# Optimization experiments

Hardware: AMD Instinct MI355X
Metric: run time of the kernel (lower is better)

Reference implementation:

```python
import jax, jax.numpy as jnp
import numpy as np

B, S, H, I, E, K = 2, 2048, 896, 4864, 4, 2


def setup_inputs() -> dict:
    key = jax.random.key(0)
    ks = jax.random.split(key, 5)
    s_h = 1.0 / np.sqrt(H)
    s_i = 1.0 / np.sqrt(I)
    return {
        "x": jax.random.normal(ks[0], (B, S, H), dtype=jnp.float32),
        # torch nn.Linear weights are [out, in]
        "router_w": jax.random.uniform(ks[1], (E, H), dtype=jnp.float32, minval=-s_h, maxval=s_h),
        "gate_w": jax.random.uniform(ks[2], (E, I, H), dtype=jnp.float32, minval=-s_h, maxval=s_h),
        "up_w": jax.random.uniform(ks[3], (E, I, H), dtype=jnp.float32, minval=-s_h, maxval=s_h),
        "down_w": jax.random.uniform(ks[4], (E, H, I), dtype=jnp.float32, minval=-s_i, maxval=s_i),
    }


def reference(x, router_w, gate_w, up_w, down_w):
    # Router: softmax in fp32, top-k, renormalize (matches torch.softmax(dtype=float) + topk)
    logits = jnp.einsum("bsh,eh->bse", x, router_w)
    probs = jax.nn.softmax(logits.astype(jnp.float32), axis=-1)
    top_w, top_i = jax.lax.top_k(probs, K)                      # [B,S,K]
    top_w = top_w / jnp.sum(top_w, axis=-1, keepdims=True)
    # Dense per-expert combine weight: zero for unselected experts
    w_full = jnp.sum(jax.nn.one_hot(top_i, E, dtype=x.dtype) * top_w[..., None].astype(x.dtype), axis=-2)  # [B,S,E]
    # All experts on all tokens (E is small); unselected get weight 0
    gate = jax.nn.silu(jnp.einsum("bsh,eih->bsei", x, gate_w))  # [B,S,E,I]
    up = jnp.einsum("bsh,eih->bsei", x, up_w)
    y = jnp.einsum("bsei,ehi->bseh", gate * up, down_w)          # [B,S,E,H]
    return jnp.einsum("bseh,bse->bsh", y, w_full)
```

## Files before the change

kernel.cpp:

```cpp
#include <hip/hip_runtime.h>
#include <hip/hip_bf16.h>

#define E_ 4
#define H_ 896
#define I_ 4864
#define T_ 4096
#define P_ 8192
#define KS2 2432

typedef unsigned short u16;
typedef __attribute__((ext_vector_type(8))) short short8;
typedef __attribute__((ext_vector_type(4))) float f32x4;

__device__ __forceinline__ void gload16(const void* g, void* l) {
  __builtin_amdgcn_global_load_lds(
      (const __attribute__((address_space(1))) unsigned int*)g,
      (__attribute__((address_space(3))) unsigned int*)l, 16, 0, 0);
}

__device__ __forceinline__ u16 f2bf(float f) {
  unsigned int u = __builtin_bit_cast(unsigned int, f);
  unsigned int r = (u + 0x7FFFu + ((u >> 16) & 1u)) >> 16;
  return (u16)r;
}

__global__ __launch_bounds__(256) void cast_bf16_kernel(const float* __restrict__ in,
                                                        u16* __restrict__ out, long n) {
  long base = ((long)blockIdx.x * 256 + threadIdx.x) * 4;
  if (base + 3 < n) {
    float4 v = *reinterpret_cast<const float4*>(in + base);
    ushort4 o;
    o.x = f2bf(v.x); o.y = f2bf(v.y); o.z = f2bf(v.z); o.w = f2bf(v.w);
    *reinterpret_cast<ushort4*>(out + base) = o;
  } else {
    for (long j = base; j < n; ++j) out[j] = f2bf(in[j]);
  }
}

__global__ __launch_bounds__(64) void router_kernel(const float* __restrict__ x,
                                                    const float* __restrict__ rw,
                                                    int* __restrict__ cnt,
                                                    int* __restrict__ pairs,
                                                    float* __restrict__ wgt) {
  int t = blockIdx.x;
  int lane = threadIdx.x;
  const float* xr = x + (long)t * H_;
  float a0 = 0.f, a1 = 0.f, a2 = 0.f, a3 = 0.f;
  for (int h = lane; h < H_; h += 64) {
    float xv = xr[h];
    a0 += xv * rw[0 * H_ + h];
    a1 += xv * rw[1 * H_ + h];
    a2 += xv * rw[2 * H_ + h];
    a3 += xv * rw[3 * H_ + h];
  }
  for (int off = 32; off > 0; off >>= 1) {
    a0 += __shfl_xor(a0, off, 64);
    a1 += __shfl_xor(a1, off, 64);
    a2 += __shfl_xor(a2, off, 64);
    a3 += __shfl_xor(a3, off, 64);
  }
  if (lane == 0) {
    float l[4] = {a0, a1, a2, a3};
    int i0 = 0;
    for (int e = 1; e < 4; ++e) if (l[e] > l[i0]) i0 = e;
    int i1 = -1;
    for (int e = 0; e < 4; ++e) {
      if (e == i0) continue;
      if (i1 < 0 || l[e] > l[i1]) i1 = e;
    }
    float w0 = 1.0f / (1.0f + __expf(l[i1] - l[i0]));
    int j0 = atomicAdd(&cnt[i0], 1);
    pairs[i0 * T_ + j0] = 2 * t;
    wgt[2 * t] = w0;
    int j1 = atomicAdd(&cnt[i1], 1);
    pairs[i1 * T_ + j1] = 2 * t + 1;
    wgt[2 * t + 1] = 1.0f - w0;
  }
}


__global__ __launch_bounds__(256, 2) void gemm1_kernel(const u16* __restrict__ xb,
                                                       const u16* __restrict__ gw,
                                                       const u16* __restrict__ uw,
                                                       const int* __restrict__ cnt,
                                                       const int* __restrict__ pairs,
                                                       u16* __restrict__ hbuf) {
  int e = blockIdx.z;
  int n = cnt[e];
  int row0 = blockIdx.y * 128;
  if (row0 >= n) return;
  int col0 = blockIdx.x * 128;

  __shared__ alignas(16) u16 As[128 * 64];
  __shared__ alignas(16) u16 Bg[128 * 64];
  __shared__ alignas(16) u16 Bu[128 * 64];
  __shared__ int rows[128];

  int tid = threadIdx.x;
  if (tid < 128) {
    int j = row0 + tid;
    if (j >= n) j = n - 1;
    rows[tid] = pairs[e * T_ + j];
  }
  __syncthreads();

  int rr = tid >> 3;
  int cc = tid & 7;
  long eoff = (long)e * I_ * H_;

  const u16* aP[4]; const u16* gP[4]; const u16* uP[4];
  u16* lA[4]; u16* lG[4]; u16* lU[4];
#pragma unroll
  for (int q = 0; q < 4; ++q) {
    int gr = rr + 32 * q;
    int g8 = (cc ^ (gr & 7)) * 8;
    aP[q] = xb + (long)(rows[gr] >> 1) * H_ + g8;
    gP[q] = gw + eoff + (long)(col0 + gr) * H_ + g8;
    uP[q] = uw + eoff + (long)(col0 + gr) * H_ + g8;
    lA[q] = As + q * 2048 + tid * 8;
    lG[q] = Bg + q * 2048 + tid * 8;
    lU[q] = Bu + q * 2048 + tid * 8;
  }

  f32x4 accg[4][4] = {};
  f32x4 accu[4][4] = {};

  int lane = tid & 63;
  int wave = tid >> 6;
  int wm = (wave >> 1) * 64;
  int wn = (wave & 1) * 64;
  int lm = lane & 15;
  int qv = lane >> 4;
  int px = qv ^ (lm & 7);

  for (int kt = 0; kt < H_; kt += 64) {
    __syncthreads();
#pragma unroll
    for (int q = 0; q < 4; ++q) {
      gload16(aP[q] + kt, lA[q]);
      gload16(gP[q] + kt, lG[q]);
      gload16(uP[q] + kt, lU[q]);
    }
    __syncthreads();

#pragma unroll
    for (int kh = 0; kh < 2; ++kh) {
      int po = (px ^ (kh << 2)) * 8;
      short8 af[4];
#pragma unroll
      for (int bi = 0; bi < 4; ++bi)
        af[bi] = *reinterpret_cast<const short8*>(&As[(wm + bi * 16 + lm) * 64 + po]);
#pragma unroll
      for (int bj = 0; bj < 4; ++bj) {
        short8 bgf = *reinterpret_cast<const short8*>(&Bg[(wn + bj * 16 + lm) * 64 + po]);
        short8 buf = *reinterpret_cast<const short8*>(&Bu[(wn + bj * 16 + lm) * 64 + po]);
#pragma unroll
        for (int bi = 0; bi < 4; ++bi) {
          accg[bi][bj] = __builtin_amdgcn_mfma_f32_16x16x32_bf16(af[bi], bgf, accg[bi][bj], 0, 0, 0);
          accu[bi][bj] = __builtin_amdgcn_mfma_f32_16x16x32_bf16(af[bi], buf, accu[bi][bj], 0, 0, 0);
        }
      }
    }
  }

  int rq = (lane >> 4) * 4;
#pragma unroll
  for (int bi = 0; bi < 4; ++bi) {
#pragma unroll
    for (int r = 0; r < 4; ++r) {
      int rloc = wm + bi * 16 + rq + r;
      if (row0 + rloc < n) {
        long p = rows[rloc];
        u16* hr = hbuf + p * (long)I_ + col0 + wn + lm;
#pragma unroll
        for (int bj = 0; bj < 4; ++bj) {
          float g = accg[bi][bj][r];
          float u = accu[bi][bj][r];
          float s = g / (1.0f + __expf(-g));
          hr[bj * 16] = f2bf(s * u);
        }
      }
    }
  }
}

__global__ __launch_bounds__(256, 3) void gemm2_kernel(const u16* __restrict__ hbuf,
                                                       const u16* __restrict__ dw,
                                                       const int* __restrict__ cnt,
                                                       const int* __restrict__ pairs,
                                                       const float* __restrict__ wgt,
                                                       float* __restrict__ out) {
  int z = blockIdx.z;
  int e = z >> 1;
  int k0 = (z & 1) * KS2;
  int n = cnt[e];
  int row0 = blockIdx.y * 128;
  if (row0 >= n) return;
  int col0 = blockIdx.x * 128;

  __shared__ alignas(16) u16 As[128 * 64];
  __shared__ alignas(16) u16 Bs[128 * 64];
  __shared__ int rows[128];

  int tid = threadIdx.x;
  if (tid < 128) {
    int j = row0 + tid;
    if (j >= n) j = n - 1;
    rows[tid] = pairs[e * T_ + j];
  }
  __syncthreads();

  int rr = tid >> 3;
  int cc = tid & 7;

  const u16* aP[4]; const u16* bP[4];
  u16* lA[4]; u16* lB[4];
#pragma unroll
  for (int q = 0; q < 4; ++q) {
    int gr = rr + 32 * q;
    int g8 = (cc ^ (gr & 7)) * 8;
    aP[q] = hbuf + (long)rows[gr] * I_ + k0 + g8;
    bP[q] = dw + (long)e * H_ * I_ + (long)(col0 + gr) * I_ + k0 + g8;
    lA[q] = As + q * 2048 + tid * 8;
    lB[q] = Bs + q * 2048 + tid * 8;
  }

  f32x4 acc[4][4] = {};

  int lane = tid & 63;
  int wave = tid >> 6;
  int wm = (wave >> 1) * 64;
  int wn = (wave & 1) * 64;
  int lm = lane & 15;
  int qv = lane >> 4;
  int px = qv ^ (lm & 7);

  for (int kt = 0; kt < KS2; kt += 64) {
    __syncthreads();
#pragma unroll
    for (int q = 0; q < 4; ++q) {
      gload16(aP[q] + kt, lA[q]);
      gload16(bP[q] + kt, lB[q]);
    }
    __syncthreads();

#pragma unroll
    for (int kh = 0; kh < 2; ++kh) {
      int po = (px ^ (kh << 2)) * 8;
      short8 af[4];
#pragma unroll
      for (int bi = 0; bi < 4; ++bi)
        af[bi] = *reinterpret_cast<const short8*>(&As[(wm + bi * 16 + lm) * 64 + po]);
#pragma unroll
      for (int bj = 0; bj < 4; ++bj) {
        short8 bf = *reinterpret_cast<const short8*>(&Bs[(wn + bj * 16 + lm) * 64 + po]);
#pragma unroll
        for (int bi = 0; bi < 4; ++bi)
          acc[bi][bj] = __builtin_amdgcn_mfma_f32_16x16x32_bf16(af[bi], bf, acc[bi][bj], 0, 0, 0);
      }
    }
  }

  int rq = (lane >> 4) * 4;
#pragma unroll
  for (int bi = 0; bi < 4; ++bi) {
#pragma unroll
    for (int r = 0; r < 4; ++r) {
      int rloc = wm + bi * 16 + rq + r;
      if (row0 + rloc < n) {
        int p = rows[rloc];
        int t = p >> 1;
        float w = wgt[p];
        float* orow = out + (long)t * H_ + col0 + wn + lm;
#pragma unroll
        for (int bj = 0; bj < 4; ++bj)
          atomicAdd(&orow[bj * 16], w * acc[bi][bj][r]);
      }
    }
  }
}

extern "C" void kernel_launch(void* const* d_in, const int* in_sizes, int n_in,
                              void* d_out, int out_size, void* d_ws, size_t ws_size,
                              hipStream_t stream) {
  const float* x        = (const float*)d_in[0];
  const float* router_w = (const float*)d_in[1];
  const float* gate_w   = (const float*)d_in[2];
  const float* up_w     = (const float*)d_in[3];
  const float* down_w   = (const float*)d_in[4];
  float* out = (float*)d_out;

  const long WN = (long)E_ * I_ * H_;

  char* ws = (char*)d_ws;
  size_t off = 0;
  auto alloc = [&](size_t bytes) {
    void* p = ws + off;
    off = (off + bytes + 255) & ~(size_t)255;
    return p;
  };
  u16* gw_b  = (u16*)alloc(WN * 2);
  u16* uw_b  = (u16*)alloc(WN * 2);
  u16* dw_b  = (u16*)alloc(WN * 2);
  u16* xb    = (u16*)alloc((long)T_ * H_ * 2);
  u16* hbuf  = (u16*)alloc((long)P_ * I_ * 2);
  int* cnt   = (int*)alloc(256);
  int* pairs = (int*)alloc((long)E_ * T_ * 4);
  float* wgt = (float*)alloc((long)P_ * 4);

  hipMemsetAsync(cnt, 0, 256, stream);
  hipMemsetAsync(d_out, 0, (size_t)out_size * sizeof(float), stream);

  cast_bf16_kernel<<<WN / 1024, 256, 0, stream>>>(gate_w, gw_b, WN);
  cast_bf16_kernel<<<WN / 1024, 256, 0, stream>>>(up_w, uw_b, WN);
  cast_bf16_kernel<<<WN / 1024, 256, 0, stream>>>(down_w, dw_b, WN);
  cast_bf16_kernel<<<((long)T_ * H_) / 1024, 256, 0, stream>>>(x, xb, (long)T_ * H_);

  router_kernel<<<T_, 64, 0, stream>>>(x, router_w, cnt, pairs, wgt);

  dim3 g1(I_ / 128, T_ / 128, E_);
  gemm1_kernel<<<g1, 256, 0, stream>>>(xb, gw_b, uw_b, cnt, pairs, hbuf);

  dim3 g2(H_ / 128, T_ / 128, E_ * 2);
  gemm2_kernel<<<g2, 256, 0, stream>>>(hbuf, dw_b, cnt, pairs, wgt, out);
}
```

Measured before the change: 659.1 us.

## Fuse weight casts, fold x cast into router, swap grid axes, replace atomics with combine

The three weight casts now run as one launch, and the activation cast moves into the router kernel. Both GEMM grids swap x and y so row tiles vary fastest, which can help weight-tile reuse in L2 and lets idle row blocks exit early. gemm2 now writes per-split, per-pair partial results into a scratch buffer reused from the gate-weight buffer, instead of issuing float atomicAdds. A new combine kernel then applies the routing weights and sums the partials. This drops the output memset and the atomic contention, at the cost of an extra pass over a large fp32 intermediate.

```diff
diff --git a/kernel.cpp b/kernel.cpp
--- a/kernel.cpp
+++ b/kernel.cpp
@@ -7,6 +7,7 @@
 #define T_ 4096
 #define P_ 8192
 #define KS2 2432
+#define WBLK 17024
 
 typedef unsigned short u16;
 typedef __attribute__((ext_vector_type(8))) short short8;
@@ -24,24 +25,28 @@
   return (u16)r;
 }
 
-__global__ __launch_bounds__(256) void cast_bf16_kernel(const float* __restrict__ in,
-                                                        u16* __restrict__ out, long n) {
-  long base = ((long)blockIdx.x * 256 + threadIdx.x) * 4;
-  if (base + 3 < n) {
-    float4 v = *reinterpret_cast<const float4*>(in + base);
-    ushort4 o;
-    o.x = f2bf(v.x); o.y = f2bf(v.y); o.z = f2bf(v.z); o.w = f2bf(v.w);
-    *reinterpret_cast<ushort4*>(out + base) = o;
-  } else {
-    for (long j = base; j < n; ++j) out[j] = f2bf(in[j]);
-  }
+__global__ __launch_bounds__(256) void cast3_kernel(const float* __restrict__ a,
+                                                    const float* __restrict__ b,
+                                                    const float* __restrict__ c,
+                                                    u16* __restrict__ oa,
+                                                    u16* __restrict__ ob,
+                                                    u16* __restrict__ oc) {
+  int wsel = blockIdx.x / WBLK;
+  long base = ((long)(blockIdx.x % WBLK) * 256 + threadIdx.x) * 4;
+  const float* in = (wsel == 0) ? a : (wsel == 1) ? b : c;
+  u16* out = (wsel == 0) ? oa : (wsel == 1) ? ob : oc;
+  float4 v = *reinterpret_cast<const float4*>(in + base);
+  ushort4 o;
+  o.x = f2bf(v.x); o.y = f2bf(v.y); o.z = f2bf(v.z); o.w = f2bf(v.w);
+  *reinterpret_cast<ushort4*>(out + base) = o;
 }
 
 __global__ __launch_bounds__(64) void router_kernel(const float* __restrict__ x,
                                                     const float* __restrict__ rw,
                                                     int* __restrict__ cnt,
                                                     int* __restrict__ pairs,
-                                                    float* __restrict__ wgt) {
+                                                    float* __restrict__ wgt,
+                                                    u16* __restrict__ xb) {
   int t = blockIdx.x;
   int lane = threadIdx.x;
   const float* xr = x + (long)t * H_;
@@ -52,6 +57,7 @@
     a1 += xv * rw[1 * H_ + h];
     a2 += xv * rw[2 * H_ + h];
     a3 += xv * rw[3 * H_ + h];
+    xb[(long)t * H_ + h] = f2bf(xv);
   }
   for (int off = 32; off > 0; off >>= 1) {
     a0 += __shfl_xor(a0, off, 64);
@@ -87,9 +93,9 @@
                                                        u16* __restrict__ hbuf) {
   int e = blockIdx.z;
   int n = cnt[e];
-  int row0 = blockIdx.y * 128;
+  int row0 = blockIdx.x * 128;
   if (row0 >= n) return;
-  int col0 = blockIdx.x * 128;
+  int col0 = blockIdx.y * 128;
 
   __shared__ alignas(16) u16 As[128 * 64];
   __shared__ alignas(16) u16 Bg[128 * 64];
@@ -188,15 +194,15 @@
                                                        const u16* __restrict__ dw,
                                                        const int* __restrict__ cnt,
                                                        const int* __restrict__ pairs,
-                                                       const float* __restrict__ wgt,
-                                                       float* __restrict__ out) {
-  int z = blockIdx.z;
-  int e = z >> 1;
-  int k0 = (z & 1) * KS2;
+                                                       float* __restrict__ ybuf) {
+  int bz = blockIdx.z;
+  int e = bz >> 1;
+  int sp = bz & 1;
+  int k0 = sp * KS2;
   int n = cnt[e];
-  int row0 = blockIdx.y * 128;
+  int row0 = blockIdx.x * 128;
   if (row0 >= n) return;
-  int col0 = blockIdx.x * 128;
+  int col0 = blockIdx.y * 128;
 
   __shared__ alignas(16) u16 As[128 * 64];
   __shared__ alignas(16) u16 Bs[128 * 64];
@@ -269,15 +275,34 @@
       int rloc = wm + bi * 16 + rq + r;
       if (row0 + rloc < n) {
         int p = rows[rloc];
-        int t = p >> 1;
-        float w = wgt[p];
-        float* orow = out + (long)t * H_ + col0 + wn + lm;
+        float* orow = ybuf + ((long)sp * P_ + p) * H_ + col0 + wn + lm;
 #pragma unroll
         for (int bj = 0; bj < 4; ++bj)
-          atomicAdd(&orow[bj * 16], w * acc[bi][bj][r]);
+          orow[bj * 16] = acc[bi][bj][r];
       }
     }
   }
+}
+
+__global__ __launch_bounds__(256) void combine_kernel(const float* __restrict__ Y,
+                                                      const float* __restrict__ wgt,
+                                                      float* __restrict__ out) {
+  long gid = (long)blockIdx.x * 256 + threadIdx.x;
+  int t = (int)(gid / 224);
+  int hc = (int)(gid % 224);
+  float w0 = wgt[2 * t];
+  float w1 = wgt[2 * t + 1];
+  const float4* y00 = reinterpret_cast<const float4*>(Y + ((long)2 * t) * H_) + hc;
+  const float4* y01 = reinterpret_cast<const float4*>(Y + ((long)P_ + 2 * t) * H_) + hc;
+  const float4* y10 = reinterpret_cast<const float4*>(Y + ((long)2 * t + 1) * H_) + hc;
+  const float4* y11 = reinterpret_cast<const float4*>(Y + ((long)P_ + 2 * t + 1) * H_) + hc;
+  float4 a = *y00, b = *y01, c = *y10, d = *y11;
+  float4 o;
+  o.x = w0 * (a.x + b.x) + w1 * (c.x + d.x);
+  o.y = w0 * (a.y + b.y) + w1 * (c.y + d.y);
+  o.z = w0 * (a.z + b.z) + w1 * (c.z + d.z);
+  o.w = w0 * (a.w + b.w) + w1 * (c.w + d.w);
+  *(reinterpret_cast<float4*>(out + (long)t * H_) + hc) = o;
 }
 
 extern "C" void kernel_launch(void* const* d_in, const int* in_sizes, int n_in,
@@ -307,20 +332,19 @@
   int* cnt   = (int*)alloc(256);
   int* pairs = (int*)alloc((long)E_ * T_ * 4);
   float* wgt = (float*)alloc((long)P_ * 4);
+  float* ybuf = (float*)gw_b;
 
   hipMemsetAsync(cnt, 0, 256, stream);
-  hipMemsetAsync(d_out, 0, (size_t)out_size * sizeof(float), stream);
-
-  cast_bf16_kernel<<<WN / 1024, 256, 0, stream>>>(gate_w, gw_b, WN);
-  cast_bf16_kernel<<<WN / 1024, 256, 0, stream>>>(up_w, uw_b, WN);
-  cast_bf16_kernel<<<WN / 1024, 256, 0, stream>>>(down_w, dw_b, WN);
-  cast_bf16_kernel<<<((long)T_ * H_) / 1024, 256, 0, stream>>>(x, xb, (long)T_ * H_);
-
-  router_kernel<<<T_, 64, 0, stream>>>(x, router_w, cnt, pairs, wgt);
-
-  dim3 g1(I_ / 128, T_ / 128, E_);
+
+  cast3_kernel<<<3 * WBLK, 256, 0, stream>>>(gate_w, up_w, down_w, gw_b, uw_b, dw_b);
+
+  router_kernel<<<T_, 64, 0, stream>>>(x, router_w, cnt, pairs, wgt, xb);
+
+  dim3 g1(T_ / 128, I_ / 128, E_);
   gemm1_kernel<<<g1, 256, 0, stream>>>(xb, gw_b, uw_b, cnt, pairs, hbuf);
 
-  dim3 g2(H_ / 128, T_ / 128, E_ * 2);
-  gemm2_kernel<<<g2, 256, 0, stream>>>(hbuf, dw_b, cnt, pairs, wgt, out);
-}
+  dim3 g2(T_ / 128, H_ / 128, E_ * 2);
+  gemm2_kernel<<<g2, 256, 0, stream>>>(hbuf, dw_b, cnt, pairs, ybuf);
+
+  combine_kernel<<<(T_ * 224) / 256, 256, 0, stream>>>(ybuf, wgt, out);
+}
```

Result: slower. 758.6 us (+15.1%).
